# Performance work log

Measured on AMD Instinct MI355X. Metric: run time of the kernel, lower is better.

Reference implementation:

```python
import jax, jax.numpy as jnp
import numpy as np

NUM_HEADS = 8


def _skew(x):
    # x: [b,h,l,m] with l == m. Pad last dim on the left, reshape, drop first row.
    b, h, l, m = x.shape
    x = jnp.pad(x, ((0, 0), (0, 0), (0, 0), (1, 0)))  # [b,h,l,m+1]
    return x.reshape(b, h, l + 1, m)[:, :, 1:, :]      # [b,h,l,m]


def _unskew(x):
    # Inverse skew: pad dim 2 on the left, reshape, drop first column.
    b, h, l, m = x.shape
    x = jnp.pad(x, ((0, 0), (0, 0), (1, 0), (0, 0)))  # [b,h,l+1,m]
    return x.reshape(b, h, l, m + 1)[:, :, :, 1:]      # [b,h,l,m]


def setup_inputs() -> dict:
    key = jax.random.key(0)
    B, L, D = 2, 2048, 512
    depth = D // NUM_HEADS
    ks = jax.random.split(key, 12)
    s = D ** -0.5
    inp = {
        "q": jax.random.normal(ks[0], (B, L, D), jnp.float32),
        "k": jax.random.normal(ks[1], (B, L, D), jnp.float32),
        "v": jax.random.normal(ks[2], (B, L, D), jnp.float32),
        # causal mask: 1 where attention is disallowed (future positions)
        "mask": (1.0 - jnp.tril(jnp.ones((L, L), jnp.float32)))[None, None],
        "wq": jax.random.normal(ks[3], (D, D), jnp.float32) * s,
        "bq": jnp.zeros((D,), jnp.float32),
        "wk": jax.random.normal(ks[4], (D, D), jnp.float32) * s,
        "bk": jnp.zeros((D,), jnp.float32),
        "wv": jax.random.normal(ks[5], (D, D), jnp.float32) * s,
        "bv": jnp.zeros((D,), jnp.float32),
        "wo": jax.random.normal(ks[6], (D, D), jnp.float32) * s,
        "bo": jnp.zeros((D,), jnp.float32),
        "key_rel": jax.random.normal(ks[7], (L, depth), jnp.float32) * (depth ** -0.5),
        "val_rel": jax.random.normal(ks[8], (L, depth), jnp.float32) * (depth ** -0.5),
    }
    return inp


def reference(q, k, v, mask, wq, bq, wk, bk, wv, bv, wo, bo, key_rel, val_rel):
    B, L, D = q.shape
    H = NUM_HEADS
    depth = D // H

    def split_heads(x):
        return x.reshape(B, L, H, depth).transpose(0, 2, 1, 3)  # [b,h,l,d]

    qh = split_heads(q @ wq + bq)
    kh = split_heads(k @ wk + bk)
    vh = split_heads(v @ wv + bv)

    logits = jnp.einsum('bhld,bhmd->bhlm', qh, kh)           # QK^T (no 1/sqrt(d) scale, per source)
    rel = _skew(jnp.einsum('bhld,md->bhlm', qh, key_rel))    # relative position logits
    logits = logits + rel + mask * (-1e9)
    aw = jax.nn.softmax(logits, axis=-1)                     # [b,h,l,m]

    out = jnp.einsum('bhlm,bhmd->bhld', aw, vh)
    rw = _unskew(aw)
    out = out + jnp.einsum('bhlm,md->bhld', rw, val_rel)

    out = out.transpose(0, 2, 1, 3).reshape(B, L, D)
    return out @ wo + bo, aw
```

## Files before the change

kernel.cpp:

```cpp
#include <hip/hip_runtime.h>
#include <hip/hip_bf16.h>


typedef __bf16 bf16;
typedef __attribute__((ext_vector_type(8))) __bf16 bf16x8;
typedef __attribute__((ext_vector_type(4))) float f32x4;

#define NL 2048
#define ND 512
#define NH 8
#define NBH 16
#define NM 4096

__device__ __forceinline__ f32x4 mfma16(bf16x8 a, bf16x8 b, f32x4 c) {
  return __builtin_amdgcn_mfma_f32_16x16x32_bf16(a, b, c, 0, 0, 0);
}

__device__ __forceinline__ void split_bf16(float x, bf16& h, bf16& l) {
  h = (bf16)x;
  l = (bf16)(x - (float)h);
}

__global__ __launch_bounds__(256) void k_prep(const float* __restrict__ key_rel,
                                              const float* __restrict__ val_rel,
                                              bf16* __restrict__ krr_h,
                                              bf16* __restrict__ krr_l,
                                              bf16* __restrict__ vrr_t) {
  int idx = blockIdx.x * 256 + threadIdx.x;
  int d = idx >> 6, dim = idx & 63;
  float kr = key_rel[(size_t)(NL - 1 - d) * 64 + dim];
  bf16 h, l;
  split_bf16(kr, h, l);
  krr_h[idx] = h;
  krr_l[idx] = l;
  float vr = val_rel[(size_t)(NL - 1 - d) * 64 + dim];
  vrr_t[(size_t)dim * NL + d] = (bf16)vr;
}

__global__ __launch_bounds__(256) void k_proj_qkv(
    const float* __restrict__ q, const float* __restrict__ k, const float* __restrict__ v,
    const float* __restrict__ wq, const float* __restrict__ bq,
    const float* __restrict__ wk, const float* __restrict__ bk,
    const float* __restrict__ wv, const float* __restrict__ bv,
    bf16* __restrict__ Qh, bf16* __restrict__ Ql,
    bf16* __restrict__ Kh, bf16* __restrict__ Kl, bf16* __restrict__ Vt) {
  __shared__ __align__(16) bf16 sAh[64][40], sAl[64][40];
  __shared__ __align__(16) bf16 sWh[64][40], sWl[64][40];

  int which = blockIdx.y >> 3;
  int n0 = (blockIdx.y & 7) << 6;
  int m0 = blockIdx.x << 6;
  const float* A  = which == 0 ? q  : (which == 1 ? k  : v);
  const float* Wp = which == 0 ? wq : (which == 1 ? wk : wv);
  const float* bias = which == 0 ? bq : (which == 1 ? bk : bv);

  int t = threadIdx.x;
  int wave = t >> 6, lane = t & 63, cl = lane & 15, g = lane >> 4;
  f32x4 acc[4] = {};

  for (int ks = 0; ks < 16; ++ks) {
    {
      int row = t >> 2, cb = (t & 3) << 3;
      const float* src = A + (size_t)(m0 + row) * ND + ks * 32 + cb;
      float4 v0 = *(const float4*)src;
      float4 v1 = *(const float4*)(src + 4);
      float vv[8] = {v0.x, v0.y, v0.z, v0.w, v1.x, v1.y, v1.z, v1.w};
      bf16x8 h8, l8;
#pragma unroll
      for (int e = 0; e < 8; ++e) { bf16 hh, ll; split_bf16(vv[e], hh, ll); h8[e] = hh; l8[e] = ll; }
      *(bf16x8*)&sAh[row][cb] = h8;
      *(bf16x8*)&sAl[row][cb] = l8;
    }
    {
      int kk = t >> 3, nb = (t & 7) << 3;
      const float* src = Wp + (size_t)(ks * 32 + kk) * ND + n0 + nb;
      float4 v0 = *(const float4*)src;
      float4 v1 = *(const float4*)(src + 4);
      float vv[8] = {v0.x, v0.y, v0.z, v0.w, v1.x, v1.y, v1.z, v1.w};
#pragma unroll
      for (int e = 0; e < 8; ++e) { bf16 hh, ll; split_bf16(vv[e], hh, ll); sWh[nb + e][kk] = hh; sWl[nb + e][kk] = ll; }
    }
    __syncthreads();
    bf16x8 ah = *(bf16x8*)&sAh[wave * 16 + cl][g * 8];
    bf16x8 al = *(bf16x8*)&sAl[wave * 16 + cl][g * 8];
#pragma unroll
    for (int c = 0; c < 4; ++c) {
      bf16x8 wh = *(bf16x8*)&sWh[c * 16 + cl][g * 8];
      bf16x8 wl = *(bf16x8*)&sWl[c * 16 + cl][g * 8];
      acc[c] = mfma16(ah, wh, acc[c]);
      acc[c] = mfma16(ah, wl, acc[c]);
      acc[c] = mfma16(al, wh, acc[c]);
    }
    __syncthreads();
  }

#pragma unroll
  for (int c = 0; c < 4; ++c) {
    int n = n0 + c * 16 + cl;
    int head = n >> 6, dim = n & 63;
    float bval = bias[n];
#pragma unroll
    for (int r = 0; r < 4; ++r) {
      int m = m0 + wave * 16 + g * 4 + r;
      int bb = m >> 11, lrow = m & 2047;
      float val = acc[c][r] + bval;
      if (which == 2) {
        Vt[((size_t)(bb * NH + head) * 64 + dim) * NL + lrow] = (bf16)val;
      } else {
        bf16 hh, ll;
        split_bf16(val, hh, ll);
        size_t off = ((size_t)(bb * NH + head) * NL + lrow) * 64 + dim;
        if (which == 0) { Qh[off] = hh; Ql[off] = ll; }
        else           { Kh[off] = hh; Kl[off] = ll; }
      }
    }
  }
}

__global__ __launch_bounds__(256) void k_attn(
    const bf16* __restrict__ Qh, const bf16* __restrict__ Ql,
    const bf16* __restrict__ Kh, const bf16* __restrict__ Kl,
    const bf16* __restrict__ Vt,
    const bf16* __restrict__ krr_h, const bf16* __restrict__ krr_l,
    const bf16* __restrict__ vrr_t,
    float* __restrict__ s_ws, bf16* __restrict__ O, float* __restrict__ aw) {
  __shared__ __align__(16) bf16 sKh[64][72], sKl[64][72];
  __shared__ __align__(16) bf16 sV[64][72];
  __shared__ __align__(16) bf16 sRh[128][72], sRl[128][72];
  __shared__ __align__(16) bf16 sVr[64][160];
  __shared__ __align__(16) bf16 sE[4][16][72];
  __shared__ __align__(16) bf16 sEb[4][16][104];
  __shared__ __align__(16) float sX[4][16][88];

  int idx = blockIdx.x;
  int qi = idx & 31;
  int bh = idx >> 5;
  if (bh >= 8) qi = 31 - qi;
  int i0 = qi << 6;

  int t = threadIdx.x;
  int wave = t >> 6, lane = t & 63, cl = lane & 15, g = lane >> 4;

  size_t qbase = ((size_t)bh * NL + (i0 + wave * 16 + cl)) * 64;
  bf16x8 qh0 = *(const bf16x8*)(Qh + qbase);
  bf16x8 qh1 = *(const bf16x8*)(Qh + qbase + 32);
  bf16x8 ql0 = *(const bf16x8*)(Ql + qbase);
  bf16x8 ql1 = *(const bf16x8*)(Ql + qbase + 32);
  qh0 = *(const bf16x8*)(Qh + qbase + g * 8);
  qh1 = *(const bf16x8*)(Qh + qbase + 32 + g * 8);
  ql0 = *(const bf16x8*)(Ql + qbase + g * 8);
  ql1 = *(const bf16x8*)(Ql + qbase + 32 + g * 8);

  f32x4 oacc[4] = {};
  float s_part[4] = {0.f, 0.f, 0.f, 0.f};

  int ntiles = qi + 1;
  for (int kt = 0; kt < ntiles; ++kt) {
    int j0 = kt << 6;
    int dmin = i0 - j0 - 63;

    {
      int row = t >> 2, cb = (t & 3) << 4;
      size_t gb = ((size_t)bh * NL + j0 + row) * 64 + cb;
      *(uint4*)&sKh[row][cb]     = *(const uint4*)(Kh + gb);
      *(uint4*)&sKh[row][cb + 8] = *(const uint4*)(Kh + gb + 8);
      *(uint4*)&sKl[row][cb]     = *(const uint4*)(Kl + gb);
      *(uint4*)&sKl[row][cb + 8] = *(const uint4*)(Kl + gb + 8);
      size_t vb = ((size_t)bh * 64 + row) * NL + j0 + cb;
      *(uint4*)&sV[row][cb]     = *(const uint4*)(Vt + vb);
      *(uint4*)&sV[row][cb + 8] = *(const uint4*)(Vt + vb + 8);
    }
    {
      int row = t >> 1, cb = (t & 1) << 5;
      int d = dmin + row;
      if (d >= 0 && d < NL) {
        const bf16* sh = krr_h + (size_t)d * 64 + cb;
        const bf16* sl = krr_l + (size_t)d * 64 + cb;
#pragma unroll
        for (int q8 = 0; q8 < 4; ++q8) {
          *(uint4*)&sRh[row][cb + q8 * 8] = *(const uint4*)(sh + q8 * 8);
          *(uint4*)&sRl[row][cb + q8 * 8] = *(const uint4*)(sl + q8 * 8);
        }
      } else {
        uint4 z = {0, 0, 0, 0};
#pragma unroll
        for (int q8 = 0; q8 < 4; ++q8) {
          *(uint4*)&sRh[row][cb + q8 * 8] = z;
          *(uint4*)&sRl[row][cb + q8 * 8] = z;
        }
      }
    }
    {
      int row = t >> 2, cb0 = (t & 3) * 40;
#pragma unroll
      for (int c8 = 0; c8 < 5; ++c8) {
        int col = cb0 + c8 * 8;
        int d0 = dmin + col;
        uint4 val;
        if (d0 >= 0 && d0 + 8 <= NL) {
          val = *(const uint4*)(vrr_t + (size_t)row * NL + d0);
        } else {
          __align__(16) bf16 tmp[8];
#pragma unroll
          for (int e = 0; e < 8; ++e) {
            int d = d0 + e;
            tmp[e] = (d >= 0 && d < NL) ? vrr_t[(size_t)row * NL + d] : (bf16)0.f;
          }
          val = *(uint4*)tmp;
        }
        *(uint4*)&sVr[row][col] = val;
      }
    }
    __syncthreads();

    {
      int r = lane >> 2, cb = (lane & 3) * 24;
      uint4 z = {0, 0, 0, 0};
      *(uint4*)&sEb[wave][r][cb] = z;
      *(uint4*)&sEb[wave][r][cb + 8] = z;
      *(uint4*)&sEb[wave][r][cb + 16] = z;
    }

#pragma unroll
    for (int xt = 0; xt < 5; ++xt) {
      int rr = wave * 16 + xt * 16 + cl;
      bf16x8 b0h = *(bf16x8*)&sRh[rr][g * 8];
      bf16x8 b0l = *(bf16x8*)&sRl[rr][g * 8];
      bf16x8 b1h = *(bf16x8*)&sRh[rr][32 + g * 8];
      bf16x8 b1l = *(bf16x8*)&sRl[rr][32 + g * 8];
      f32x4 xa = {};
      xa = mfma16(qh0, b0h, xa);
      xa = mfma16(qh1, b1h, xa);
      xa = mfma16(qh0, b0l, xa);
      xa = mfma16(qh1, b1l, xa);
      xa = mfma16(ql0, b0h, xa);
      xa = mfma16(ql1, b1h, xa);
#pragma unroll
      for (int r = 0; r < 4; ++r) sX[wave][g * 4 + r][xt * 16 + cl] = xa[r];
    }

#pragma unroll
    for (int c = 0; c < 4; ++c) {
      int rr = c * 16 + cl;
      bf16x8 k0h = *(bf16x8*)&sKh[rr][g * 8];
      bf16x8 k0l = *(bf16x8*)&sKl[rr][g * 8];
      bf16x8 k1h = *(bf16x8*)&sKh[rr][32 + g * 8];
      bf16x8 k1l = *(bf16x8*)&sKl[rr][32 + g * 8];
      f32x4 la = {};
      la = mfma16(qh0, k0h, la);
      la = mfma16(qh1, k1h, la);
      la = mfma16(qh0, k0l, la);
      la = mfma16(qh1, k1l, la);
      la = mfma16(ql0, k0h, la);
      la = mfma16(ql1, k1h, la);
#pragma unroll
      for (int r = 0; r < 4; ++r) {
        int lr = g * 4 + r;
        int irow = i0 + wave * 16 + lr;
        int j = j0 + c * 16 + cl;
        float e = 0.f;
        if (j <= irow) e = __expf(la[r] + sX[wave][lr][lr - c * 16 - cl + 63]);
        s_part[r] += e;
        bf16 eb = (bf16)e;
        sE[wave][lr][c * 16 + cl] = eb;
        sEb[wave][lr][lr + 63 - c * 16 - cl] = eb;
      }
    }

#pragma unroll
    for (int dt = 0; dt < 4; ++dt) {
#pragma unroll
      for (int ks = 0; ks < 2; ++ks) {
        bf16x8 ea = *(bf16x8*)&sE[wave][cl][ks * 32 + g * 8];
        bf16x8 vb = *(bf16x8*)&sV[dt * 16 + cl][ks * 32 + g * 8];
        oacc[dt] = mfma16(ea, vb, oacc[dt]);
      }
#pragma unroll
      for (int ks = 0; ks < 3; ++ks) {
        bf16x8 ea = *(bf16x8*)&sEb[wave][cl][ks * 32 + g * 8];
        bf16x8 vb = *(bf16x8*)&sVr[dt * 16 + cl][wave * 16 + ks * 32 + g * 8];
        oacc[dt] = mfma16(ea, vb, oacc[dt]);
      }
    }

    {
      int rr = lane >> 2, cb = (lane & 3) << 4;
      char* p = (char*)aw + ((size_t)bh * NL + i0 + wave * 16 + rr) * 8192 + 4096 + 2 * (j0 + cb);
      *(uint4*)p = *(uint4*)&sE[wave][rr][cb];
      *(uint4*)(p + 16) = *(uint4*)&sE[wave][rr][cb + 8];
    }
    __syncthreads();
  }

#pragma unroll
  for (int r = 0; r < 4; ++r) {
    float vsum = s_part[r];
    vsum += __shfl_xor(vsum, 1);
    vsum += __shfl_xor(vsum, 2);
    vsum += __shfl_xor(vsum, 4);
    vsum += __shfl_xor(vsum, 8);
    s_part[r] = vsum;
  }
  if (cl == 0) {
#pragma unroll
    for (int r = 0; r < 4; ++r)
      s_ws[(size_t)bh * NL + i0 + wave * 16 + g * 4 + r] = s_part[r];
  }
  int bb = bh >> 3, hh = bh & 7;
#pragma unroll
  for (int r = 0; r < 4; ++r) {
    float inv = 1.f / s_part[r];
    int irow = i0 + wave * 16 + g * 4 + r;
    size_t obase = (size_t)(bb * NL + irow) * ND + hh * 64;
#pragma unroll
    for (int dt = 0; dt < 4; ++dt)
      O[obase + dt * 16 + cl] = (bf16)(oacc[dt][r] * inv);
  }
}

__global__ __launch_bounds__(256) void k_rescale(const float* __restrict__ s_ws,
                                                 float* __restrict__ aw) {
  int row = blockIdx.x;
  int i = row & 2047;
  int Wc = ((i >> 6) + 1) << 6;
  float inv = 1.f / s_ws[row];
  int t = threadIdx.x;
  const char* ebase = (const char*)(aw + (size_t)row * NL) + 4096;
  uint4 epack = {0, 0, 0, 0};
  if (t * 8 < Wc) epack = *(const uint4*)(ebase + 16 * t);
  __syncthreads();
  bf16x8 ev = *(bf16x8*)&epack;
  __align__(16) float vals[8];
#pragma unroll
  for (int e = 0; e < 8; ++e) {
    int j = t * 8 + e;
    vals[e] = (j <= i) ? (float)ev[e] * inv : 0.f;
  }
  float* dst = aw + (size_t)row * NL + t * 8;
  *(float4*)dst = *(float4*)&vals[0];
  *(float4*)(dst + 4) = *(float4*)&vals[4];
}

__global__ __launch_bounds__(256) void k_oproj(const bf16* __restrict__ O,
                                               const float* __restrict__ wo,
                                               const float* __restrict__ bo,
                                               float* __restrict__ out) {
  __shared__ __align__(16) bf16 sA[64][40];
  __shared__ __align__(16) bf16 sW[64][40];
  int m0 = blockIdx.x << 6, n0 = blockIdx.y << 6;
  int t = threadIdx.x;
  int wave = t >> 6, lane = t & 63, cl = lane & 15, g = lane >> 4;
  f32x4 acc[4] = {};
  for (int ks = 0; ks < 16; ++ks) {
    {
      int row = t >> 2, cb = (t & 3) << 3;
      *(uint4*)&sA[row][cb] = *(const uint4*)(O + (size_t)(m0 + row) * ND + ks * 32 + cb);
    }
    {
      int kk = t >> 3, nb = (t & 7) << 3;
      const float* src = wo + (size_t)(ks * 32 + kk) * ND + n0 + nb;
      float4 v0 = *(const float4*)src;
      float4 v1 = *(const float4*)(src + 4);
      float vv[8] = {v0.x, v0.y, v0.z, v0.w, v1.x, v1.y, v1.z, v1.w};
#pragma unroll
      for (int e = 0; e < 8; ++e) sW[nb + e][kk] = (bf16)vv[e];
    }
    __syncthreads();
    bf16x8 a = *(bf16x8*)&sA[wave * 16 + cl][g * 8];
#pragma unroll
    for (int c = 0; c < 4; ++c) {
      bf16x8 b = *(bf16x8*)&sW[c * 16 + cl][g * 8];
      acc[c] = mfma16(a, b, acc[c]);
    }
    __syncthreads();
  }
#pragma unroll
  for (int c = 0; c < 4; ++c) {
    int n = n0 + c * 16 + cl;
    float bval = bo[n];
#pragma unroll
    for (int r = 0; r < 4; ++r)
      out[(size_t)(m0 + wave * 16 + g * 4 + r) * ND + n] = acc[c][r] + bval;
  }
}

extern "C" void kernel_launch(void* const* d_in, const int* in_sizes, int n_in,
                              void* d_out, int out_size, void* d_ws, size_t ws_size,
                              hipStream_t stream) {
  const float* q  = (const float*)d_in[0];
  const float* k  = (const float*)d_in[1];
  const float* v  = (const float*)d_in[2];
  const float* wq = (const float*)d_in[4];
  const float* bq = (const float*)d_in[5];
  const float* wk = (const float*)d_in[6];
  const float* bk = (const float*)d_in[7];
  const float* wv = (const float*)d_in[8];
  const float* bv = (const float*)d_in[9];
  const float* wo = (const float*)d_in[10];
  const float* bo = (const float*)d_in[11];
  const float* key_rel = (const float*)d_in[12];
  const float* val_rel = (const float*)d_in[13];

  char* ws = (char*)d_ws;
  const size_t SZ = 4194304;
  bf16* Qh = (bf16*)(ws + 0 * SZ);
  bf16* Ql = (bf16*)(ws + 1 * SZ);
  bf16* Kh = (bf16*)(ws + 2 * SZ);
  bf16* Kl = (bf16*)(ws + 3 * SZ);
  bf16* Vt = (bf16*)(ws + 4 * SZ);
  bf16* O  = (bf16*)(ws + 5 * SZ);
  bf16* krr_h = (bf16*)(ws + 6 * SZ);
  bf16* krr_l = (bf16*)(ws + 6 * SZ + 262144);
  bf16* vrr_t = (bf16*)(ws + 6 * SZ + 2 * 262144);
  float* s_ws = (float*)(ws + 6 * SZ + 3 * 262144);

  float* out = (float*)d_out;
  float* aw = out + (size_t)NM * ND;

  k_prep<<<dim3(512), dim3(256), 0, stream>>>(key_rel, val_rel, krr_h, krr_l, vrr_t);
  k_proj_qkv<<<dim3(64, 24), dim3(256), 0, stream>>>(q, k, v, wq, bq, wk, bk, wv, bv,
                                                     Qh, Ql, Kh, Kl, Vt);
  k_attn<<<dim3(512), dim3(256), 0, stream>>>(Qh, Ql, Kh, Kl, Vt, krr_h, krr_l, vrr_t,
                                              s_ws, O, aw);
  k_rescale<<<dim3(32768), dim3(256), 0, stream>>>(s_ws, aw);
  k_oproj<<<dim3(64, 8), dim3(256), 0, stream>>>(O, wo, bo, out);
}
```

Before: 648.3 us.

## Split relative-key logits into separate GEMM kernel writing skewed fp16 scratch

```diff
diff --git a/kernel.cpp b/kernel.cpp
--- a/kernel.cpp
+++ b/kernel.cpp
@@ -3,13 +3,13 @@
 
 
 typedef __bf16 bf16;
+typedef _Float16 f16;
 typedef __attribute__((ext_vector_type(8))) __bf16 bf16x8;
 typedef __attribute__((ext_vector_type(4))) float f32x4;
 
 #define NL 2048
 #define ND 512
 #define NH 8
-#define NBH 16
 #define NM 4096
 
 __device__ __forceinline__ f32x4 mfma16(bf16x8 a, bf16x8 b, f32x4 c) {
@@ -117,20 +117,12 @@
   }
 }
 
-__global__ __launch_bounds__(256) void k_attn(
+__global__ __launch_bounds__(256) void k_xgemm(
     const bf16* __restrict__ Qh, const bf16* __restrict__ Ql,
-    const bf16* __restrict__ Kh, const bf16* __restrict__ Kl,
-    const bf16* __restrict__ Vt,
     const bf16* __restrict__ krr_h, const bf16* __restrict__ krr_l,
-    const bf16* __restrict__ vrr_t,
-    float* __restrict__ s_ws, bf16* __restrict__ O, float* __restrict__ aw) {
-  __shared__ __align__(16) bf16 sKh[64][72], sKl[64][72];
-  __shared__ __align__(16) bf16 sV[64][72];
-  __shared__ __align__(16) bf16 sRh[128][72], sRl[128][72];
-  __shared__ __align__(16) bf16 sVr[64][160];
-  __shared__ __align__(16) bf16 sE[4][16][72];
-  __shared__ __align__(16) bf16 sEb[4][16][104];
-  __shared__ __align__(16) float sX[4][16][88];
+    float* __restrict__ aw) {
+  __shared__ __align__(16) bf16 sRh[64][72], sRl[64][72];
+  __shared__ __align__(16) f16 sT[64][72];
 
   int idx = blockIdx.x;
   int qi = idx & 31;
@@ -142,88 +134,25 @@
   int wave = t >> 6, lane = t & 63, cl = lane & 15, g = lane >> 4;
 
   size_t qbase = ((size_t)bh * NL + (i0 + wave * 16 + cl)) * 64;
-  bf16x8 qh0 = *(const bf16x8*)(Qh + qbase);
-  bf16x8 qh1 = *(const bf16x8*)(Qh + qbase + 32);
-  bf16x8 ql0 = *(const bf16x8*)(Ql + qbase);
-  bf16x8 ql1 = *(const bf16x8*)(Ql + qbase + 32);
-  qh0 = *(const bf16x8*)(Qh + qbase + g * 8);
-  qh1 = *(const bf16x8*)(Qh + qbase + 32 + g * 8);
-  ql0 = *(const bf16x8*)(Ql + qbase + g * 8);
-  ql1 = *(const bf16x8*)(Ql + qbase + 32 + g * 8);
-
-  f32x4 oacc[4] = {};
-  float s_part[4] = {0.f, 0.f, 0.f, 0.f};
-
-  int ntiles = qi + 1;
-  for (int kt = 0; kt < ntiles; ++kt) {
-    int j0 = kt << 6;
-    int dmin = i0 - j0 - 63;
-
+  bf16x8 qh0 = *(const bf16x8*)(Qh + qbase + g * 8);
+  bf16x8 qh1 = *(const bf16x8*)(Qh + qbase + 32 + g * 8);
+  bf16x8 ql0 = *(const bf16x8*)(Ql + qbase + g * 8);
+  bf16x8 ql1 = *(const bf16x8*)(Ql + qbase + 32 + g * 8);
+
+  for (int kt = 0; kt <= qi; ++kt) {
+    int d0 = kt << 6;
     {
       int row = t >> 2, cb = (t & 3) << 4;
-      size_t gb = ((size_t)bh * NL + j0 + row) * 64 + cb;
-      *(uint4*)&sKh[row][cb]     = *(const uint4*)(Kh + gb);
-      *(uint4*)&sKh[row][cb + 8] = *(const uint4*)(Kh + gb + 8);
-      *(uint4*)&sKl[row][cb]     = *(const uint4*)(Kl + gb);
-      *(uint4*)&sKl[row][cb + 8] = *(const uint4*)(Kl + gb + 8);
-      size_t vb = ((size_t)bh * 64 + row) * NL + j0 + cb;
-      *(uint4*)&sV[row][cb]     = *(const uint4*)(Vt + vb);
-      *(uint4*)&sV[row][cb + 8] = *(const uint4*)(Vt + vb + 8);
-    }
-    {
-      int row = t >> 1, cb = (t & 1) << 5;
-      int d = dmin + row;
-      if (d >= 0 && d < NL) {
-        const bf16* sh = krr_h + (size_t)d * 64 + cb;
-        const bf16* sl = krr_l + (size_t)d * 64 + cb;
-#pragma unroll
-        for (int q8 = 0; q8 < 4; ++q8) {
-          *(uint4*)&sRh[row][cb + q8 * 8] = *(const uint4*)(sh + q8 * 8);
-          *(uint4*)&sRl[row][cb + q8 * 8] = *(const uint4*)(sl + q8 * 8);
-        }
-      } else {
-        uint4 z = {0, 0, 0, 0};
-#pragma unroll
-        for (int q8 = 0; q8 < 4; ++q8) {
-          *(uint4*)&sRh[row][cb + q8 * 8] = z;
-          *(uint4*)&sRl[row][cb + q8 * 8] = z;
-        }
-      }
-    }
-    {
-      int row = t >> 2, cb0 = (t & 3) * 40;
-#pragma unroll
-      for (int c8 = 0; c8 < 5; ++c8) {
-        int col = cb0 + c8 * 8;
-        int d0 = dmin + col;
-        uint4 val;
-        if (d0 >= 0 && d0 + 8 <= NL) {
-          val = *(const uint4*)(vrr_t + (size_t)row * NL + d0);
-        } else {
-          __align__(16) bf16 tmp[8];
-#pragma unroll
-          for (int e = 0; e < 8; ++e) {
-            int d = d0 + e;
-            tmp[e] = (d >= 0 && d < NL) ? vrr_t[(size_t)row * NL + d] : (bf16)0.f;
-          }
-          val = *(uint4*)tmp;
-        }
-        *(uint4*)&sVr[row][col] = val;
-      }
-    }
-    __syncthreads();
-
-    {
-      int r = lane >> 2, cb = (lane & 3) * 24;
-      uint4 z = {0, 0, 0, 0};
-      *(uint4*)&sEb[wave][r][cb] = z;
-      *(uint4*)&sEb[wave][r][cb + 8] = z;
-      *(uint4*)&sEb[wave][r][cb + 16] = z;
-    }
-
-#pragma unroll
-    for (int xt = 0; xt < 5; ++xt) {
-      int rr = wave * 16 + xt * 16 + cl;
+      size_t gb = (size_t)(d0 + row) * 64 + cb;
+      *(uint4*)&sRh[row][cb]     = *(const uint4*)(krr_h + gb);
+      *(uint4*)&sRh[row][cb + 8] = *(const uint4*)(krr_h + gb + 8);
+      *(uint4*)&sRl[row][cb]     = *(const uint4*)(krr_l + gb);
+      *(uint4*)&sRl[row][cb + 8] = *(const uint4*)(krr_l + gb + 8);
+    }
+    __syncthreads();
+#pragma unroll
+    for (int c = 0; c < 4; ++c) {
+      int rr = c * 16 + cl;
       bf16x8 b0h = *(bf16x8*)&sRh[rr][g * 8];
       bf16x8 b0l = *(bf16x8*)&sRl[rr][g * 8];
       bf16x8 b1h = *(bf16x8*)&sRh[rr][32 + g * 8];
@@ -236,7 +165,104 @@
       xa = mfma16(ql0, b0h, xa);
       xa = mfma16(ql1, b1h, xa);
 #pragma unroll
-      for (int r = 0; r < 4; ++r) sX[wave][g * 4 + r][xt * 16 + cl] = xa[r];
+      for (int r = 0; r < 4; ++r)
+        sT[wave * 16 + g * 4 + r][c * 16 + cl] = (f16)xa[r];
+    }
+    __syncthreads();
+#pragma unroll
+    for (int it = 0; it < 16; ++it) {
+      int row = it * 4 + (t >> 6), col = t & 63;
+      int irow = i0 + row;
+      int j = irow - d0 - col;
+      if (j >= 0) {
+        f16* dst = (f16*)((char*)aw + ((size_t)bh * NL + irow) * 8192);
+        dst[j] = sT[row][col];
+      }
+    }
+  }
+}
+
+__global__ __launch_bounds__(256) void k_attn(
+    const bf16* __restrict__ Qh, const bf16* __restrict__ Ql,
+    const bf16* __restrict__ Kh, const bf16* __restrict__ Kl,
+    const bf16* __restrict__ Vt, const bf16* __restrict__ vrr_t,
+    float* __restrict__ s_ws, bf16* __restrict__ O, float* __restrict__ aw) {
+  __shared__ __align__(16) bf16 sKh[64][72], sKl[64][72];
+  __shared__ __align__(16) bf16 sV[64][72];
+  __shared__ __align__(16) f16 sXs[64][72];
+  __shared__ __align__(16) bf16 sVr[64][160];
+  __shared__ __align__(16) bf16 sE[4][16][72];
+  __shared__ __align__(16) bf16 sEb[4][16][104];
+
+  int idx = blockIdx.x;
+  int qi = idx & 31;
+  int bh = idx >> 5;
+  if (bh >= 8) qi = 31 - qi;
+  int i0 = qi << 6;
+
+  int t = threadIdx.x;
+  int wave = t >> 6, lane = t & 63, cl = lane & 15, g = lane >> 4;
+
+  size_t qbase = ((size_t)bh * NL + (i0 + wave * 16 + cl)) * 64;
+  bf16x8 qh0 = *(const bf16x8*)(Qh + qbase + g * 8);
+  bf16x8 qh1 = *(const bf16x8*)(Qh + qbase + 32 + g * 8);
+  bf16x8 ql0 = *(const bf16x8*)(Ql + qbase + g * 8);
+  bf16x8 ql1 = *(const bf16x8*)(Ql + qbase + 32 + g * 8);
+
+  f32x4 oacc[4] = {};
+  float s_part[4] = {0.f, 0.f, 0.f, 0.f};
+
+  int ntiles = qi + 1;
+  for (int kt = 0; kt < ntiles; ++kt) {
+    int j0 = kt << 6;
+    int dmin = i0 - j0 - 63;
+
+    {
+      int row = t >> 2, cb = (t & 3) << 4;
+      size_t gb = ((size_t)bh * NL + j0 + row) * 64 + cb;
+      *(uint4*)&sKh[row][cb]     = *(const uint4*)(Kh + gb);
+      *(uint4*)&sKh[row][cb + 8] = *(const uint4*)(Kh + gb + 8);
+      *(uint4*)&sKl[row][cb]     = *(const uint4*)(Kl + gb);
+      *(uint4*)&sKl[row][cb + 8] = *(const uint4*)(Kl + gb + 8);
+      size_t vb = ((size_t)bh * 64 + row) * NL + j0 + cb;
+      *(uint4*)&sV[row][cb]     = *(const uint4*)(Vt + vb);
+      *(uint4*)&sV[row][cb + 8] = *(const uint4*)(Vt + vb + 8);
+    }
+    {
+      int row = t >> 2, cb = (t & 3) << 4;
+      const char* src = (const char*)aw + ((size_t)bh * NL + i0 + row) * 8192 + 2 * (j0 + cb);
+      *(uint4*)&sXs[row][cb]     = *(const uint4*)src;
+      *(uint4*)&sXs[row][cb + 8] = *(const uint4*)(src + 16);
+    }
+    {
+      int row = t >> 2, cb0 = (t & 3) * 40;
+#pragma unroll
+      for (int c8 = 0; c8 < 5; ++c8) {
+        int col = cb0 + c8 * 8;
+        int d0 = dmin + col;
+        uint4 val;
+        if (d0 >= 0 && d0 + 8 <= NL) {
+          val = *(const uint4*)(vrr_t + (size_t)row * NL + d0);
+        } else {
+          __align__(16) bf16 tmp[8];
+#pragma unroll
+          for (int e = 0; e < 8; ++e) {
+            int d = d0 + e;
+            tmp[e] = (d >= 0 && d < NL) ? vrr_t[(size_t)row * NL + d] : (bf16)0.f;
+          }
+          val = *(uint4*)tmp;
+        }
+        *(uint4*)&sVr[row][col] = val;
+      }
+    }
+    __syncthreads();
+
+    {
+      int r = lane >> 2, cb = (lane & 3) * 24;
+      uint4 z = {0, 0, 0, 0};
+      *(uint4*)&sEb[wave][r][cb] = z;
+      *(uint4*)&sEb[wave][r][cb + 8] = z;
+      *(uint4*)&sEb[wave][r][cb + 16] = z;
     }
 
 #pragma unroll
@@ -259,7 +285,10 @@
         int irow = i0 + wave * 16 + lr;
         int j = j0 + c * 16 + cl;
         float e = 0.f;
-        if (j <= irow) e = __expf(la[r] + sX[wave][lr][lr - c * 16 - cl + 63]);
+        if (j <= irow) {
+          float X = (float)sXs[wave * 16 + lr][c * 16 + cl];
+          e = __expf(la[r] + X);
+        }
         s_part[r] += e;
         bf16 eb = (bf16)e;
         sE[wave][lr][c * 16 + cl] = eb;
@@ -420,8 +449,8 @@
   k_prep<<<dim3(512), dim3(256), 0, stream>>>(key_rel, val_rel, krr_h, krr_l, vrr_t);
   k_proj_qkv<<<dim3(64, 24), dim3(256), 0, stream>>>(q, k, v, wq, bq, wk, bk, wv, bv,
                                                      Qh, Ql, Kh, Kl, Vt);
-  k_attn<<<dim3(512), dim3(256), 0, stream>>>(Qh, Ql, Kh, Kl, Vt, krr_h, krr_l, vrr_t,
-                                              s_ws, O, aw);
+  k_xgemm<<<dim3(512), dim3(256), 0, stream>>>(Qh, Ql, krr_h, krr_l, aw);
+  k_attn<<<dim3(512), dim3(256), 0, stream>>>(Qh, Ql, Kh, Kl, Vt, vrr_t, s_ws, O, aw);
   k_rescale<<<dim3(32768), dim3(256), 0, stream>>>(s_ws, aw);
   k_oproj<<<dim3(64, 8), dim3(256), 0, stream>>>(O, wo, bo, out);
 }
```

Result: faster. 606.2 us (-6.5%).
